# Kernel optimization log

Hardware: AMD Instinct MI355X
Metric: run time of the kernel (lower is better)

Reference implementation:

```python
import jax, jax.numpy as jnp
import numpy as np

G, N_PER, H, F_IN, E = 512, 128, 128, 133, 524288
K1, K2, K3 = 103, 83, 67  # ceil(0.8*n) chain: 128->103->83->67 (PyG TopKPooling ratio=0.8)
NEG = 0.01   # leaky_relu default slope
EPS = 1e-5   # BatchNorm eps


def setup_inputs() -> dict:
    key = jax.random.key(0)
    ks = jax.random.split(key, 16)
    e_per = E // G
    # edges are intra-graph: local endpoints + per-graph offset
    src_l = jax.random.randint(ks[0], (G, e_per), 0, N_PER)
    dst_l = jax.random.randint(ks[1], (G, e_per), 0, N_PER)
    off = (jnp.arange(G) * N_PER)[:, None]
    src = (src_l + off).reshape(-1).astype(jnp.int32)
    dst = (dst_l + off).reshape(-1).astype(jnp.int32)
    batch = jnp.repeat(jnp.arange(G, dtype=jnp.int32), N_PER)

    def rn(k, shape, scale=0.05):
        return jax.random.normal(k, shape, dtype=jnp.float32) * scale

    return dict(
        x=jax.random.normal(ks[2], (G * N_PER, F_IN), dtype=jnp.float32),
        src=src, dst=dst, batch=batch,
        W1=rn(ks[3], (F_IN, H)), b1=jnp.zeros((H,), jnp.float32),
        W2=rn(ks[4], (H, H)), b2=jnp.zeros((H,), jnp.float32),
        W3=rn(ks[5], (H, H)), b3=jnp.zeros((H,), jnp.float32),
        p1=rn(ks[6], (H,), 0.1), p2=rn(ks[7], (H,), 0.1), p3=rn(ks[8], (H,), 0.1),
        lin1_W=rn(ks[9], (2 * H, 1024)), lin1_b=jnp.zeros((1024,), jnp.float32),
        lin2_W=rn(ks[10], (1024, 64)), lin2_b=jnp.zeros((64,), jnp.float32),
        lin3_W=rn(ks[11], (64, 2)), lin3_b=jnp.zeros((2,), jnp.float32),
        bn1_g=jnp.ones((1024,), jnp.float32), bn1_b=jnp.zeros((1024,), jnp.float32),
        bn1_rm=jnp.zeros((1024,), jnp.float32), bn1_rv=jnp.ones((1024,), jnp.float32),
        bn2_g=jnp.ones((64,), jnp.float32), bn2_b=jnp.zeros((64,), jnp.float32),
        bn2_rm=jnp.zeros((64,), jnp.float32), bn2_rv=jnp.ones((64,), jnp.float32),
    )


def _gcn(x, W, b, src, dst, em, n_nodes):
    # GCNConv with self-loops & symmetric norm; em masks edges removed by pooling.
    deg = jax.ops.segment_sum(em, dst, num_segments=n_nodes) + 1.0  # +1 self loop
    dis = jax.lax.rsqrt(deg)
    h = x @ W
    coef = dis[src] * dis[dst] * em                      # [E]
    agg = jax.ops.segment_sum(h[src] * coef[:, None], dst, num_segments=n_nodes)
    return agg + h * (1.0 / deg)[:, None] + b            # self-loop term: deg_i^-1 * h_i


def _topk(x, p, src, dst, em, n_per, k):
    # TopKPooling: score = x@p/||p||, keep top-k per graph, gate by tanh(score).
    g = x.shape[0] // n_per
    score = (x @ p) / jnp.linalg.norm(p)                 # [g*n_per]
    vals, idx = jax.lax.top_k(score.reshape(g, n_per), k)  # [g,k]
    xk = jnp.take_along_axis(x.reshape(g, n_per, -1), idx[:, :, None], axis=1)
    x_new = (xk * jnp.tanh(vals)[:, :, None]).reshape(g * k, -1)
    # remap surviving edges; drop (mask) edges touching removed nodes
    remap = jnp.full((g * n_per,), -1, jnp.int32)
    gperm = (jnp.arange(g, dtype=jnp.int32)[:, None] * n_per + idx.astype(jnp.int32)).reshape(-1)
    remap = remap.at[gperm].set(jnp.arange(g * k, dtype=jnp.int32))
    s2, d2 = remap[src], remap[dst]
    ok = (s2 >= 0) & (d2 >= 0)
    return x_new, jnp.where(ok, s2, 0), jnp.where(ok, d2, 0), em * ok.astype(em.dtype)


def _readout(x, g):
    xg = x.reshape(g, -1, x.shape[-1])
    return jnp.concatenate([xg.max(axis=1), xg.mean(axis=1)], axis=-1)  # [g, 2H]


def _lrelu(v):
    return jax.nn.leaky_relu(v, NEG)


def _bn(v, gam, bet, rm, rv):  # eval-mode BatchNorm1d (running stats)
    return (v - rm) * jax.lax.rsqrt(rv + EPS) * gam + bet


def _forward(x, src, dst, W1, b1, W2, b2, W3, b3, p1, p2, p3,
             lin1_W, lin1_b, lin2_W, lin2_b, lin3_W, lin3_b,
             bn1_g, bn1_b, bn1_rm, bn1_rv, bn2_g, bn2_b, bn2_rm, bn2_rv):
    em = jnp.ones(src.shape, jnp.float32)
    h = _lrelu(_gcn(x, W1, b1, src, dst, em, G * N_PER))
    h, src, dst, em = _topk(h, p1, src, dst, em, N_PER, K1)
    r1 = _readout(h, G)
    h = _lrelu(_gcn(h, W2, b2, src, dst, em, G * K1))
    h, src, dst, em = _topk(h, p2, src, dst, em, K1, K2)
    r2 = _readout(h, G)
    h = _lrelu(_gcn(h, W3, b3, src, dst, em, G * K2))
    h, src, dst, em = _topk(h, p3, src, dst, em, K2, K3)
    r3 = _readout(h, G)
    z = r1 + r2 + r3                                      # [G, 2H]
    z = _bn(_lrelu(z @ lin1_W + lin1_b), bn1_g, bn1_b, bn1_rm, bn1_rv)
    z = _bn(_lrelu(z @ lin2_W + lin2_b), bn2_g, bn2_b, bn2_rm, bn2_rv)
    # dropout p=0.5 is identity in eval mode
    return z @ lin3_W + lin3_b                            # [G, num_classes]


def reference(x, src, dst, batch, W1, b1, W2, b2, W3, b3, p1, p2, p3,
              lin1_W, lin1_b, lin2_W, lin2_b, lin3_W, lin3_b,
              bn1_g, bn1_b, bn1_rm, bn1_rv, bn2_g, bn2_b, bn2_rm, bn2_rv):
    # batch is implicit in the regular [G, n_per] layout; kept for signature parity.
    return _forward(x, src, dst, W1, b1, W2, b2, W3, b3, p1, p2, p3,
                    lin1_W, lin1_b, lin2_W, lin2_b, lin3_W, lin3_b,
                    bn1_g, bn1_b, bn1_rm, bn1_rv, bn2_g, bn2_b, bn2_rm, bn2_rv)
```

## Files before the change

### kernel.cpp

```cpp
#include <hip/hip_runtime.h>

#define NEGS 0.01f
#define BNEPS 1e-5f

typedef short bf16x8 __attribute__((ext_vector_type(8)));
typedef float f32x4 __attribute__((ext_vector_type(4)));

__device__ __forceinline__ void split2(float v, short& hi, short& lo) {
    unsigned u = __float_as_uint(v);
    unsigned r = (u + 0x7FFFu + ((u >> 16) & 1u)) >> 16;
    hi = (short)r;
    float hf = __uint_as_float(r << 16);
    float l = v - hf;
    unsigned ul = __float_as_uint(l);
    lo = (short)((ul + 0x7FFFu + ((ul >> 16) & 1u)) >> 16);
}

__global__ __launch_bounds__(256) void split_all(
    const float* __restrict__ W1, const float* __restrict__ W2,
    const float* __restrict__ W3, const float* __restrict__ L1,
    short* __restrict__ h1, short* __restrict__ l1,
    short* __restrict__ h2, short* __restrict__ l2,
    short* __restrict__ h3, short* __restrict__ l3,
    short* __restrict__ h4, short* __restrict__ l4)
{
    int idx = blockIdx.x * 256 + threadIdx.x;
    const float* B; short *H, *L; int K, N, K32, loc;
    if (idx < 20480)      { B = W1; H = h1; L = l1; K = 133; N = 128;  K32 = 160; loc = idx; }
    else if (idx < 36864) { B = W2; H = h2; L = l2; K = 128; N = 128;  K32 = 128; loc = idx - 20480; }
    else if (idx < 53248) { B = W3; H = h3; L = l3; K = 128; N = 128;  K32 = 128; loc = idx - 36864; }
    else                  { B = L1; H = h4; L = l4; K = 256; N = 1024; K32 = 256; loc = idx - 53248; }
    int n = loc % N, k = loc / N;
    float v = (k < K) ? B[(long)k * N + n] : 0.f;
    short hi, lo; split2(v, hi, lo);
    H[(long)n * K32 + k] = hi;
    L[(long)n * K32 + k] = lo;
}

template<int KCH, int VEC, int EPI>
__global__ __launch_bounds__(256) void mfma_gemm(
    const float* __restrict__ A, const short* __restrict__ Bh_t,
    const short* __restrict__ Bl_t, float* __restrict__ C,
    int M, int N, int K,
    const float* __restrict__ bias, const float* __restrict__ bng,
    const float* __restrict__ bnb, const float* __restrict__ bnrm,
    const float* __restrict__ bnrv)
{
    constexpr int K32 = KCH * 32;
    __shared__ short Ahs[64 * 40], Als[64 * 40];
    __shared__ short Bhs[128 * 40], Bls[128 * 40];

    const int tid = threadIdx.x;
    const int bm = blockIdx.y * 64, bn = blockIdx.x * 128;
    const int lane = tid & 63, w = tid >> 6, wm = w >> 1, wn = w & 1;
    const int lm = lane & 15, lk = (lane >> 4) * 8;

    const int arow = tid >> 2, akl = (tid & 3) * 8;
    const int brow = tid & 127, bhl = tid >> 7;
    const short* bsrc = bhl ? Bl_t : Bh_t;
    short* bdst = bhl ? Bls : Bhs;

    const f32x4 zz = {0.f, 0.f, 0.f, 0.f};
    f32x4 acc[2][4];
#pragma unroll
    for (int i = 0; i < 2; ++i)
#pragma unroll
        for (int j = 0; j < 4; ++j) acc[i][j] = zz;

    for (int c = 0; c < KCH; ++c) {
        float av[8];
        if constexpr (VEC == 4) {
            const float4 v0 = *(const float4*)&A[(long)(bm + arow) * K + c * 32 + akl];
            const float4 v1 = *(const float4*)&A[(long)(bm + arow) * K + c * 32 + akl + 4];
            av[0] = v0.x; av[1] = v0.y; av[2] = v0.z; av[3] = v0.w;
            av[4] = v1.x; av[5] = v1.y; av[6] = v1.z; av[7] = v1.w;
        } else {
#pragma unroll
            for (int j = 0; j < 8; ++j) {
                int k = c * 32 + akl + j;
                av[j] = (k < K) ? A[(long)(bm + arow) * K + k] : 0.f;
            }
        }
        bf16x8 h8, l8;
#pragma unroll
        for (int j = 0; j < 8; ++j) { short h_, l_; split2(av[j], h_, l_); h8[j] = h_; l8[j] = l_; }
        *(bf16x8*)&Ahs[arow * 40 + akl] = h8;
        *(bf16x8*)&Als[arow * 40 + akl] = l8;
        const long bbase = (long)(bn + brow) * K32 + c * 32;
#pragma unroll
        for (int j = 0; j < 4; ++j)
            *(bf16x8*)&bdst[brow * 40 + j * 8] = *(const bf16x8*)&bsrc[bbase + j * 8];
        __syncthreads();

        bf16x8 ah0 = *(const bf16x8*)&Ahs[(wm * 32 + lm) * 40 + lk];
        bf16x8 ah1 = *(const bf16x8*)&Ahs[(wm * 32 + 16 + lm) * 40 + lk];
        bf16x8 al0 = *(const bf16x8*)&Als[(wm * 32 + lm) * 40 + lk];
        bf16x8 al1 = *(const bf16x8*)&Als[(wm * 32 + 16 + lm) * 40 + lk];
#pragma unroll
        for (int nt = 0; nt < 4; ++nt) {
            bf16x8 bh = *(const bf16x8*)&Bhs[(wn * 64 + nt * 16 + lm) * 40 + lk];
            bf16x8 bl = *(const bf16x8*)&Bls[(wn * 64 + nt * 16 + lm) * 40 + lk];
            acc[0][nt] = __builtin_amdgcn_mfma_f32_16x16x32_bf16(ah0, bh, acc[0][nt], 0, 0, 0);
            acc[1][nt] = __builtin_amdgcn_mfma_f32_16x16x32_bf16(ah1, bh, acc[1][nt], 0, 0, 0);
            acc[0][nt] = __builtin_amdgcn_mfma_f32_16x16x32_bf16(ah0, bl, acc[0][nt], 0, 0, 0);
            acc[1][nt] = __builtin_amdgcn_mfma_f32_16x16x32_bf16(ah1, bl, acc[1][nt], 0, 0, 0);
            acc[0][nt] = __builtin_amdgcn_mfma_f32_16x16x32_bf16(al0, bh, acc[0][nt], 0, 0, 0);
            acc[1][nt] = __builtin_amdgcn_mfma_f32_16x16x32_bf16(al1, bh, acc[1][nt], 0, 0, 0);
        }
        __syncthreads();
    }

#pragma unroll
    for (int mt = 0; mt < 2; ++mt) {
        int r0 = bm + wm * 32 + mt * 16 + (lane >> 4) * 4;
#pragma unroll
        for (int nt = 0; nt < 4; ++nt) {
            int col = bn + wn * 64 + nt * 16 + lm;
            float bi = 0.f, sc_ = 1.f, rm_ = 0.f, bb_ = 0.f;
            if (EPI == 1) {
                bi = bias[col];
                sc_ = (1.0f / sqrtf(bnrv[col] + BNEPS)) * bng[col];
                rm_ = bnrm[col]; bb_ = bnb[col];
            }
#pragma unroll
            for (int r = 0; r < 4; ++r) {
                float v = acc[mt][nt][r];
                if (EPI == 1) {
                    v += bi;
                    v = v >= 0.f ? v : NEGS * v;
                    v = (v - rm_) * sc_ + bb_;
                }
                C[(long)(r0 + r) * N + col] = v;
            }
        }
    }
}

template<int NC, int KK, bool FIRST, bool LAST, bool ACCUM>
__global__ __launch_bounds__(1024, 8) void gcn_topk(
    const float* __restrict__ h_pre,
    const int* __restrict__ srcIn, const int* __restrict__ dstIn,
    int* ePK,
    const float* __restrict__ bias, const float* __restrict__ p,
    float* __restrict__ x_new,
    float* __restrict__ z)
{
    __shared__ float h_s[NC][128];
    __shared__ float2 csr[1024];
    __shared__ int   head[NC];
    __shared__ float deg_s[NC], dis_s[NC], invd_s[NC];
    __shared__ float sc[128];
    __shared__ int   id[128];
    __shared__ float gate[KK];
    __shared__ float b_s[128], p_s[128];
    __shared__ int   remap_l[NC];
    __shared__ float pnorm;

    const int g = blockIdx.x, tid = threadIdx.x, lane = tid & 63;
    const float NINF = -__builtin_inff();
    constexpr int NITER = (NC + 7) / 8;

    int es_r, ed_r; bool live;
    {
        int eg = g * 1024 + tid;
        if (FIRST) { es_r = srcIn[eg] & 127; ed_r = dstIn[eg] & 127; live = true; }
        else       { int pk = ePK[eg]; es_r = pk & 127; ed_r = (pk >> 7) & 127; live = (pk >> 14) != 0; }
    }

    {
        const float4* hp = (const float4*)(h_pre + (long)g * NC * 128);
        float4* h4 = (float4*)&h_s[0][0];
        for (int i = tid; i < NC * 32; i += 1024) h4[i] = hp[i];
    }
    if (tid < 128) { b_s[tid] = bias[tid]; p_s[tid] = p[tid]; sc[tid] = 0.f; }
    for (int i = tid; i < NC; i += 1024) { deg_s[i] = 1.f; head[i] = 0; }
    __syncthreads();

    if (tid < 64) {
        float s = p_s[tid] * p_s[tid] + p_s[tid + 64] * p_s[tid + 64];
#pragma unroll
        for (int o = 32; o; o >>= 1) s += __shfl_xor(s, o, 64);
        if (tid == 0) pnorm = sqrtf(s);
    }
    if (live) {
        atomicAdd(&deg_s[ed_r], 1.0f);
        atomicAdd(&head[ed_r], 1);
    }
    __syncthreads();

    for (int i = tid; i < NC; i += 1024) {
        float d = deg_s[i];
        dis_s[i] = 1.0f / sqrtf(d);
        invd_s[i] = 1.0f / d;
    }
    if (tid < 64) {
        int c0 = head[tid];
        int c1 = (tid + 64 < NC) ? head[tid + 64] : 0;
        int s0 = c0, s1 = c1;
#pragma unroll
        for (int o = 1; o < 64; o <<= 1) { int t = __shfl_up(s0, o, 64); if (lane >= o) s0 += t; }
        int tot0 = __shfl(s0, 63, 64);
#pragma unroll
        for (int o = 1; o < 64; o <<= 1) { int t = __shfl_up(s1, o, 64); if (lane >= o) s1 += t; }
        s1 += tot0;
        head[tid] = s0 - c0;
        if (tid + 64 < NC) head[tid + 64] = s1 - c1;
    }
    __syncthreads();

    if (live) {
        int slot = atomicAdd(&head[ed_r], 1);
        csr[slot] = make_float2(__int_as_float(es_r), dis_s[es_r] * dis_s[ed_r]);
    }
    __syncthreads();

    float va[NITER];
    {
        const int f = tid & 127, grp = tid >> 7;
#pragma unroll
        for (int i = 0; i < NITER; ++i) {
            int nd = grp + i * 8;
            if (nd < NC) {
                int kb = nd ? head[nd - 1] : 0;
                int ke = head[nd];
                float acc = 0.f;
                for (int k = kb; k < ke; ++k) {
                    float2 rec = csr[k];
                    acc += h_s[__float_as_int(rec.x)][f] * rec.y;
                }
                float v = acc + h_s[nd][f] * invd_s[nd] + b_s[f];
                v = v >= 0.f ? v : NEGS * v;
                va[i] = v;
                float ps = v * p_s[f];
#pragma unroll
                for (int o = 32; o; o >>= 1) ps += __shfl_xor(ps, o, 64);
                if (lane == 0) atomicAdd(&sc[nd], ps);
            }
        }
    }
    __syncthreads();

    {
        const int f = tid & 127, grp = tid >> 7;
#pragma unroll
        for (int i = 0; i < NITER; ++i) {
            int nd = grp + i * 8;
            if (nd < NC) h_s[nd][f] = va[i];
        }
    }
    __syncthreads();

    if (tid < 128) {
        if (tid < NC) { sc[tid] = sc[tid] / pnorm; id[tid] = tid; }
        else          { sc[tid] = NINF; id[tid] = 0x7fffffff; }
    }
    __syncthreads();

    if (tid < 64) {
        for (int size = 2; size <= 128; size <<= 1) {
            for (int stride = size >> 1; stride > 0; stride >>= 1) {
                int i = 2 * stride * (tid / stride) + (tid % stride);
                int j = i + stride;
                float si_ = sc[i], sj_ = sc[j];
                int ii = id[i], ij = id[j];
                bool iFirst = (si_ > sj_) || (si_ == sj_ && ii < ij);
                bool descRegion = ((i & size) == 0);
                bool doSwap = descRegion ? !iFirst : iFirst;
                if (doSwap) { sc[i] = sj_; sc[j] = si_; id[i] = ij; id[j] = ii; }
                __asm__ volatile("" ::: "memory");
            }
        }
    }
    __syncthreads();

    for (int j = tid; j < KK; j += 1024) gate[j] = tanhf(sc[j]);
    if constexpr (!LAST) {
        for (int i = tid; i < NC; i += 1024) remap_l[i] = -1;
    }
    __syncthreads();
    if constexpr (!LAST) {
        for (int j = tid; j < KK; j += 1024) remap_l[id[j]] = j;
    }
    __syncthreads();

    if constexpr (!LAST) {
        int s2 = remap_l[es_r], d2 = remap_l[ed_r];
        bool ok = (s2 >= 0) && (d2 >= 0);
        int lv = (live && ok) ? 1 : 0;
        ePK[g * 1024 + tid] = (ok ? s2 : 0) | ((ok ? d2 : 0) << 7) | (lv << 14);
    }

    float* pmax = (float*)&csr[0];
    float* psum = pmax + 1024;
    {
        const int f = tid & 127, jj = tid >> 7;
        float rmx = NINF, rsm = 0.f;
        for (int j = jj; j < KK; j += 8) {
            float v = h_s[id[j]][f] * gate[j];
            if constexpr (!LAST) x_new[((long)g * KK + j) * 128 + f] = v;
            rmx = fmaxf(rmx, v);
            rsm += v;
        }
        pmax[jj * 128 + f] = rmx; psum[jj * 128 + f] = rsm;
    }
    __syncthreads();

    if (tid < 128) {
        float m = pmax[tid], s = psum[tid];
#pragma unroll
        for (int jj = 1; jj < 8; ++jj) { m = fmaxf(m, pmax[jj * 128 + tid]); s += psum[jj * 128 + tid]; }
        float mean = s / (float)KK;
        if constexpr (ACCUM) {
            z[g * 256 + tid] += m;
            z[g * 256 + 128 + tid] += mean;
        } else {
            z[g * 256 + tid] = m;
            z[g * 256 + 128 + tid] = mean;
        }
    }
}

__global__ __launch_bounds__(256) void mlp_tail(
    const float* __restrict__ t1,
    const float* __restrict__ W2, const float* __restrict__ b2v,
    const float* __restrict__ g2, const float* __restrict__ bb2,
    const float* __restrict__ rm2, const float* __restrict__ rv2,
    const float* __restrict__ W3, const float* __restrict__ b3v,
    float* __restrict__ out)
{
    __shared__ float t1s[1024];
    __shared__ float part[4][64];
    __shared__ float t2s[64];
    const int row = blockIdx.x, tid = threadIdx.x;

    for (int i = tid; i < 1024; i += 256) t1s[i] = t1[(long)row * 1024 + i];
    __syncthreads();

    int c = tid & 63, seg = tid >> 6;
    float s = 0.f;
    for (int k = seg * 256; k < seg * 256 + 256; ++k)
        s = fmaf(t1s[k], W2[k * 64 + c], s);
    part[seg][c] = s;
    __syncthreads();

    if (tid < 64) {
        float v = part[0][c] + part[1][c] + part[2][c] + part[3][c] + b2v[c];
        v = v >= 0.f ? v : NEGS * v;
        v = (v - rm2[c]) * (1.0f / sqrtf(rv2[c] + BNEPS)) * g2[c] + bb2[c];
        t2s[c] = v;
    }
    __syncthreads();

    if (tid < 128) {
        int cc = tid >> 6, k = tid & 63;
        float prod = t2s[k] * W3[k * 2 + cc];
#pragma unroll
        for (int o = 32; o; o >>= 1) prod += __shfl_xor(prod, o, 64);
        if (k == 0) out[row * 2 + cc] = prod + b3v[cc];
    }
}

extern "C" void kernel_launch(void* const* d_in, const int* in_sizes, int n_in,
                              void* d_out, int out_size, void* d_ws, size_t ws_size,
                              hipStream_t stream)
{
    const float* x    = (const float*)d_in[0];
    const int*   src  = (const int*)d_in[1];
    const int*   dst  = (const int*)d_in[2];
    const float* W1   = (const float*)d_in[4];
    const float* b1   = (const float*)d_in[5];
    const float* W2   = (const float*)d_in[6];
    const float* b2   = (const float*)d_in[7];
    const float* W3   = (const float*)d_in[8];
    const float* b3   = (const float*)d_in[9];
    const float* p1   = (const float*)d_in[10];
    const float* p2   = (const float*)d_in[11];
    const float* p3   = (const float*)d_in[12];
    const float* l1W  = (const float*)d_in[13];
    const float* l1b  = (const float*)d_in[14];
    const float* l2W  = (const float*)d_in[15];
    const float* l2b  = (const float*)d_in[16];
    const float* l3W  = (const float*)d_in[17];
    const float* l3b  = (const float*)d_in[18];
    const float* bn1g = (const float*)d_in[19];
    const float* bn1b = (const float*)d_in[20];
    const float* bn1rm= (const float*)d_in[21];
    const float* bn1rv= (const float*)d_in[22];
    const float* bn2g = (const float*)d_in[23];
    const float* bn2b = (const float*)d_in[24];
    const float* bn2rm= (const float*)d_in[25];
    const float* bn2rv= (const float*)d_in[26];
    float* out = (float*)d_out;

    float* ws = (float*)d_ws;
    size_t o = 0;
    float* h_pre = ws + o; o += 65536L * 128;
    float* x_cur = ws + o; o += 52736L * 128;
    float* z     = ws + o; o += 512L * 256;
    float* t1    = ws + o; o += 512L * 1024;
    int*   ePK   = (int*)(ws + o); o += 524288;
    short* sp = (short*)(ws + o);
    short* h1s = sp;
    short* l1s = h1s + 20480;
    short* h2s = l1s + 20480;
    short* l2s = h2s + 16384;
    short* h3s = l2s + 16384;
    short* l3s = h3s + 16384;
    short* h4s = l3s + 16384;
    short* l4s = h4s + 262144;

    split_all<<<1232, 256, 0, stream>>>(W1, W2, W3, l1W,
        h1s, l1s, h2s, l2s, h3s, l3s, h4s, l4s);

    mfma_gemm<5,1,0><<<dim3(1,1024), 256, 0, stream>>>(
        x, h1s, l1s, h_pre, 65536, 128, 133, nullptr, nullptr, nullptr, nullptr, nullptr);
    gcn_topk<128,103,true,false,false><<<512, 1024, 0, stream>>>(
        h_pre, src, dst, ePK, b1, p1, x_cur, z);

    mfma_gemm<4,4,0><<<dim3(1,824), 256, 0, stream>>>(
        x_cur, h2s, l2s, h_pre, 52736, 128, 128, nullptr, nullptr, nullptr, nullptr, nullptr);
    gcn_topk<103,83,false,false,true><<<512, 1024, 0, stream>>>(
        h_pre, nullptr, nullptr, ePK, b2, p2, x_cur, z);

    mfma_gemm<4,4,0><<<dim3(1,664), 256, 0, stream>>>(
        x_cur, h3s, l3s, h_pre, 42496, 128, 128, nullptr, nullptr, nullptr, nullptr, nullptr);
    gcn_topk<83,67,false,true,true><<<512, 1024, 0, stream>>>(
        h_pre, nullptr, nullptr, ePK, b3, p3, nullptr, z);

    mfma_gemm<8,4,1><<<dim3(8,8), 256, 0, stream>>>(
        z, h4s, l4s, t1, 512, 1024, 256, l1b, bn1g, bn1b, bn1rm, bn1rv);
    mlp_tail<<<512, 256, 0, stream>>>(
        t1, l2W, l2b, bn2g, bn2b, bn2rm, bn2rv, l3W, l3b, out);
}
```

Measured before the change: 296.5 us.

## Keep B weights resident in LDS and load A directly into MFMA registers; vectorize GCN aggregation

The GEMM is restructured so each block loads the whole split-bf16 B panel for its 128 columns into shared memory once. Each wave then reads its A rows straight from global memory into MFMA operand registers, which removes the per-K-chunk A staging through LDS and the two barriers per chunk, and the block tile grows to 128x128. In gcn_topk, the aggregation and pooling loops move to float4 per thread with 32 nodes in flight. The atomicAdd score update becomes a direct store, and the max/sum readout reduction reuses h_s. The costs are higher register pressure from 16 accumulators per wave, more LDS for the full K panel, and uncoalesced-per-lane global A loads.

```diff
diff --git a/kernel.cpp b/kernel.cpp
--- a/kernel.cpp
+++ b/kernel.cpp
@@ -37,87 +37,85 @@
     L[(long)n * K32 + k] = lo;
 }
 
-template<int KCH, int VEC, int EPI>
-__global__ __launch_bounds__(256) void mfma_gemm(
+template<int K, int K32, int EPI>
+__global__ __launch_bounds__(256) void gemm_bres(
     const float* __restrict__ A, const short* __restrict__ Bh_t,
-    const short* __restrict__ Bl_t, float* __restrict__ C,
-    int M, int N, int K,
+    const short* __restrict__ Bl_t, float* __restrict__ C, int N,
     const float* __restrict__ bias, const float* __restrict__ bng,
     const float* __restrict__ bnb, const float* __restrict__ bnrm,
     const float* __restrict__ bnrv)
 {
-    constexpr int K32 = KCH * 32;
-    __shared__ short Ahs[64 * 40], Als[64 * 40];
-    __shared__ short Bhs[128 * 40], Bls[128 * 40];
+    constexpr int KP = K32 + 8;
+    constexpr int NKS = K32 / 32;
+    __shared__ short Bhs[128 * KP];
+    __shared__ short Bls[128 * KP];
 
     const int tid = threadIdx.x;
-    const int bm = blockIdx.y * 64, bn = blockIdx.x * 128;
-    const int lane = tid & 63, w = tid >> 6, wm = w >> 1, wn = w & 1;
+    const int bm = blockIdx.x * 128, n0 = blockIdx.y * 128;
+    const int lane = tid & 63, w = tid >> 6;
     const int lm = lane & 15, lk = (lane >> 4) * 8;
 
-    const int arow = tid >> 2, akl = (tid & 3) * 8;
-    const int brow = tid & 127, bhl = tid >> 7;
-    const short* bsrc = bhl ? Bl_t : Bh_t;
-    short* bdst = bhl ? Bls : Bhs;
+    for (int i = tid; i < 128 * (K32 / 8); i += 256) {
+        int n = i / (K32 / 8), kb = (i % (K32 / 8)) * 8;
+        *(bf16x8*)&Bhs[n * KP + kb] = *(const bf16x8*)&Bh_t[(long)(n0 + n) * K32 + kb];
+        *(bf16x8*)&Bls[n * KP + kb] = *(const bf16x8*)&Bl_t[(long)(n0 + n) * K32 + kb];
+    }
+    __syncthreads();
 
     const f32x4 zz = {0.f, 0.f, 0.f, 0.f};
-    f32x4 acc[2][4];
+    f32x4 acc[2][8];
 #pragma unroll
     for (int i = 0; i < 2; ++i)
 #pragma unroll
-        for (int j = 0; j < 4; ++j) acc[i][j] = zz;
-
-    for (int c = 0; c < KCH; ++c) {
-        float av[8];
-        if constexpr (VEC == 4) {
-            const float4 v0 = *(const float4*)&A[(long)(bm + arow) * K + c * 32 + akl];
-            const float4 v1 = *(const float4*)&A[(long)(bm + arow) * K + c * 32 + akl + 4];
-            av[0] = v0.x; av[1] = v0.y; av[2] = v0.z; av[3] = v0.w;
-            av[4] = v1.x; av[5] = v1.y; av[6] = v1.z; av[7] = v1.w;
-        } else {
+        for (int j = 0; j < 8; ++j) acc[i][j] = zz;
+
+    const int r0 = bm + w * 32;
+    for (int ks = 0; ks < NKS; ++ks) {
+        const int k0 = ks * 32 + lk;
+        bf16x8 ah[2], al[2];
+#pragma unroll
+        for (int mt = 0; mt < 2; ++mt) {
+            const long rowb = (long)(r0 + mt * 16 + lm) * K;
+            float av[8];
+            if constexpr (K % 4 == 0) {
+                const float4 v0 = *(const float4*)&A[rowb + k0];
+                const float4 v1 = *(const float4*)&A[rowb + k0 + 4];
+                av[0] = v0.x; av[1] = v0.y; av[2] = v0.z; av[3] = v0.w;
+                av[4] = v1.x; av[5] = v1.y; av[6] = v1.z; av[7] = v1.w;
+            } else {
+#pragma unroll
+                for (int j = 0; j < 8; ++j) {
+                    int kk = k0 + j;
+                    av[j] = (kk < K) ? A[rowb + kk] : 0.f;
+                }
+            }
 #pragma unroll
             for (int j = 0; j < 8; ++j) {
-                int k = c * 32 + akl + j;
-                av[j] = (k < K) ? A[(long)(bm + arow) * K + k] : 0.f;
-            }
-        }
-        bf16x8 h8, l8;
-#pragma unroll
-        for (int j = 0; j < 8; ++j) { short h_, l_; split2(av[j], h_, l_); h8[j] = h_; l8[j] = l_; }
-        *(bf16x8*)&Ahs[arow * 40 + akl] = h8;
-        *(bf16x8*)&Als[arow * 40 + akl] = l8;
-        const long bbase = (long)(bn + brow) * K32 + c * 32;
-#pragma unroll
-        for (int j = 0; j < 4; ++j)
-            *(bf16x8*)&bdst[brow * 40 + j * 8] = *(const bf16x8*)&bsrc[bbase + j * 8];
-        __syncthreads();
-
-        bf16x8 ah0 = *(const bf16x8*)&Ahs[(wm * 32 + lm) * 40 + lk];
-        bf16x8 ah1 = *(const bf16x8*)&Ahs[(wm * 32 + 16 + lm) * 40 + lk];
-        bf16x8 al0 = *(const bf16x8*)&Als[(wm * 32 + lm) * 40 + lk];
-        bf16x8 al1 = *(const bf16x8*)&Als[(wm * 32 + 16 + lm) * 40 + lk];
-#pragma unroll
-        for (int nt = 0; nt < 4; ++nt) {
-            bf16x8 bh = *(const bf16x8*)&Bhs[(wn * 64 + nt * 16 + lm) * 40 + lk];
-            bf16x8 bl = *(const bf16x8*)&Bls[(wn * 64 + nt * 16 + lm) * 40 + lk];
-            acc[0][nt] = __builtin_amdgcn_mfma_f32_16x16x32_bf16(ah0, bh, acc[0][nt], 0, 0, 0);
-            acc[1][nt] = __builtin_amdgcn_mfma_f32_16x16x32_bf16(ah1, bh, acc[1][nt], 0, 0, 0);
-            acc[0][nt] = __builtin_amdgcn_mfma_f32_16x16x32_bf16(ah0, bl, acc[0][nt], 0, 0, 0);
-            acc[1][nt] = __builtin_amdgcn_mfma_f32_16x16x32_bf16(ah1, bl, acc[1][nt], 0, 0, 0);
-            acc[0][nt] = __builtin_amdgcn_mfma_f32_16x16x32_bf16(al0, bh, acc[0][nt], 0, 0, 0);
-            acc[1][nt] = __builtin_amdgcn_mfma_f32_16x16x32_bf16(al1, bh, acc[1][nt], 0, 0, 0);
-        }
-        __syncthreads();
+                short h_, l_; split2(av[j], h_, l_);
+                ah[mt][j] = h_; al[mt][j] = l_;
+            }
+        }
+#pragma unroll
+        for (int nt = 0; nt < 8; ++nt) {
+            bf16x8 bh = *(const bf16x8*)&Bhs[(nt * 16 + lm) * KP + k0];
+            bf16x8 bl = *(const bf16x8*)&Bls[(nt * 16 + lm) * KP + k0];
+#pragma unroll
+            for (int mt = 0; mt < 2; ++mt) {
+                acc[mt][nt] = __builtin_amdgcn_mfma_f32_16x16x32_bf16(ah[mt], bh, acc[mt][nt], 0, 0, 0);
+                acc[mt][nt] = __builtin_amdgcn_mfma_f32_16x16x32_bf16(ah[mt], bl, acc[mt][nt], 0, 0, 0);
+                acc[mt][nt] = __builtin_amdgcn_mfma_f32_16x16x32_bf16(al[mt], bh, acc[mt][nt], 0, 0, 0);
+            }
+        }
     }
 
 #pragma unroll
     for (int mt = 0; mt < 2; ++mt) {
-        int r0 = bm + wm * 32 + mt * 16 + (lane >> 4) * 4;
-#pragma unroll
-        for (int nt = 0; nt < 4; ++nt) {
-            int col = bn + wn * 64 + nt * 16 + lm;
+        const int row0 = r0 + mt * 16 + (lane >> 4) * 4;
+#pragma unroll
+        for (int nt = 0; nt < 8; ++nt) {
+            const int col = n0 + nt * 16 + lm;
             float bi = 0.f, sc_ = 1.f, rm_ = 0.f, bb_ = 0.f;
-            if (EPI == 1) {
+            if constexpr (EPI == 1) {
                 bi = bias[col];
                 sc_ = (1.0f / sqrtf(bnrv[col] + BNEPS)) * bng[col];
                 rm_ = bnrm[col]; bb_ = bnb[col];
@@ -125,12 +123,12 @@
 #pragma unroll
             for (int r = 0; r < 4; ++r) {
                 float v = acc[mt][nt][r];
-                if (EPI == 1) {
+                if constexpr (EPI == 1) {
                     v += bi;
                     v = v >= 0.f ? v : NEGS * v;
                     v = (v - rm_) * sc_ + bb_;
                 }
-                C[(long)(r0 + r) * N + col] = v;
+                C[(long)(row0 + r) * N + col] = v;
             }
         }
     }
@@ -157,8 +155,10 @@
     __shared__ float pnorm;
 
     const int g = blockIdx.x, tid = threadIdx.x, lane = tid & 63;
+    const int f4 = (tid & 31) * 4;
+    const int grp = tid >> 5;
     const float NINF = -__builtin_inff();
-    constexpr int NITER = (NC + 7) / 8;
+    constexpr int NIT4 = (NC + 31) / 32;
 
     int es_r, ed_r; bool live;
     {
@@ -172,7 +172,7 @@
         float4* h4 = (float4*)&h_s[0][0];
         for (int i = tid; i < NC * 32; i += 1024) h4[i] = hp[i];
     }
-    if (tid < 128) { b_s[tid] = bias[tid]; p_s[tid] = p[tid]; sc[tid] = 0.f; }
+    if (tid < 128) { b_s[tid] = bias[tid]; p_s[tid] = p[tid]; }
     for (int i = tid; i < NC; i += 1024) { deg_s[i] = 1.f; head[i] = 0; }
     __syncthreads();
 
@@ -214,39 +214,51 @@
     }
     __syncthreads();
 
-    float va[NITER];
-    {
-        const int f = tid & 127, grp = tid >> 7;
-#pragma unroll
-        for (int i = 0; i < NITER; ++i) {
-            int nd = grp + i * 8;
-            if (nd < NC) {
-                int kb = nd ? head[nd - 1] : 0;
-                int ke = head[nd];
-                float acc = 0.f;
-                for (int k = kb; k < ke; ++k) {
-                    float2 rec = csr[k];
-                    acc += h_s[__float_as_int(rec.x)][f] * rec.y;
-                }
-                float v = acc + h_s[nd][f] * invd_s[nd] + b_s[f];
-                v = v >= 0.f ? v : NEGS * v;
-                va[i] = v;
-                float ps = v * p_s[f];
-#pragma unroll
-                for (int o = 32; o; o >>= 1) ps += __shfl_xor(ps, o, 64);
-                if (lane == 0) atomicAdd(&sc[nd], ps);
-            }
-        }
-    }
-    __syncthreads();
-
-    {
-        const int f = tid & 127, grp = tid >> 7;
-#pragma unroll
-        for (int i = 0; i < NITER; ++i) {
-            int nd = grp + i * 8;
-            if (nd < NC) h_s[nd][f] = va[i];
-        }
+    const float4 p4 = *(const float4*)&p_s[f4];
+    const float4 b4 = *(const float4*)&b_s[f4];
+    float4 va[NIT4];
+#pragma unroll
+    for (int i = 0; i < NIT4; ++i) {
+        int nd = grp + i * 32;
+        if ((NC & 31) == 0 || nd < NC) {
+            int kb = nd ? head[nd - 1] : 0;
+            int ke = head[nd];
+            float4 acc = make_float4(0.f, 0.f, 0.f, 0.f);
+            for (int k = kb; k < ke; ++k) {
+                float2 rec = csr[k];
+                const float4 hv = *(const float4*)&h_s[__float_as_int(rec.x)][f4];
+                acc.x = fmaf(hv.x, rec.y, acc.x);
+                acc.y = fmaf(hv.y, rec.y, acc.y);
+                acc.z = fmaf(hv.z, rec.y, acc.z);
+                acc.w = fmaf(hv.w, rec.y, acc.w);
+            }
+            const float4 h0 = *(const float4*)&h_s[nd][f4];
+            const float iv = invd_s[nd];
+            float4 v;
+            v.x = acc.x + h0.x * iv + b4.x;
+            v.y = acc.y + h0.y * iv + b4.y;
+            v.z = acc.z + h0.z * iv + b4.z;
+            v.w = acc.w + h0.w * iv + b4.w;
+            v.x = v.x >= 0.f ? v.x : NEGS * v.x;
+            v.y = v.y >= 0.f ? v.y : NEGS * v.y;
+            v.z = v.z >= 0.f ? v.z : NEGS * v.z;
+            v.w = v.w >= 0.f ? v.w : NEGS * v.w;
+            va[i] = v;
+            float ps = v.x * p4.x + v.y * p4.y + v.z * p4.z + v.w * p4.w;
+            ps += __shfl_xor(ps, 16, 64);
+            ps += __shfl_xor(ps, 8, 64);
+            ps += __shfl_xor(ps, 4, 64);
+            ps += __shfl_xor(ps, 2, 64);
+            ps += __shfl_xor(ps, 1, 64);
+            if ((tid & 31) == 0) sc[nd] = ps;
+        }
+    }
+    __syncthreads();
+
+#pragma unroll
+    for (int i = 0; i < NIT4; ++i) {
+        int nd = grp + i * 32;
+        if ((NC & 31) == 0 || nd < NC) *(float4*)&h_s[nd][f4] = va[i];
     }
     __syncthreads();
 
@@ -290,25 +302,41 @@
         ePK[g * 1024 + tid] = (ok ? s2 : 0) | ((ok ? d2 : 0) << 7) | (lv << 14);
     }
 
-    float* pmax = (float*)&csr[0];
-    float* psum = pmax + 1024;
     {
-        const int f = tid & 127, jj = tid >> 7;
-        float rmx = NINF, rsm = 0.f;
-        for (int j = jj; j < KK; j += 8) {
-            float v = h_s[id[j]][f] * gate[j];
-            if constexpr (!LAST) x_new[((long)g * KK + j) * 128 + f] = v;
-            rmx = fmaxf(rmx, v);
-            rsm += v;
-        }
-        pmax[jj * 128 + f] = rmx; psum[jj * 128 + f] = rsm;
+        const int jj = tid >> 5;
+        float4 rmx = make_float4(NINF, NINF, NINF, NINF);
+        float4 rsm = make_float4(0.f, 0.f, 0.f, 0.f);
+        for (int j = jj; j < KK; j += 32) {
+            const float gt = gate[j];
+            const float4 hv = *(const float4*)&h_s[id[j]][f4];
+            float4 v;
+            v.x = hv.x * gt; v.y = hv.y * gt; v.z = hv.z * gt; v.w = hv.w * gt;
+            if constexpr (!LAST) *(float4*)&x_new[((long)g * KK + j) * 128 + f4] = v;
+            rmx.x = fmaxf(rmx.x, v.x); rmx.y = fmaxf(rmx.y, v.y);
+            rmx.z = fmaxf(rmx.z, v.z); rmx.w = fmaxf(rmx.w, v.w);
+            rsm.x += v.x; rsm.y += v.y; rsm.z += v.z; rsm.w += v.w;
+        }
+        rmx.x = fmaxf(rmx.x, __shfl_xor(rmx.x, 32, 64));
+        rmx.y = fmaxf(rmx.y, __shfl_xor(rmx.y, 32, 64));
+        rmx.z = fmaxf(rmx.z, __shfl_xor(rmx.z, 32, 64));
+        rmx.w = fmaxf(rmx.w, __shfl_xor(rmx.w, 32, 64));
+        rsm.x += __shfl_xor(rsm.x, 32, 64);
+        rsm.y += __shfl_xor(rsm.y, 32, 64);
+        rsm.z += __shfl_xor(rsm.z, 32, 64);
+        rsm.w += __shfl_xor(rsm.w, 32, 64);
+        __syncthreads();
+        if (lane < 32) {
+            const int w = tid >> 6;
+            *(float4*)&h_s[w][f4] = rmx;
+            *(float4*)&h_s[16 + w][f4] = rsm;
+        }
     }
     __syncthreads();
 
     if (tid < 128) {
-        float m = pmax[tid], s = psum[tid];
-#pragma unroll
-        for (int jj = 1; jj < 8; ++jj) { m = fmaxf(m, pmax[jj * 128 + tid]); s += psum[jj * 128 + tid]; }
+        float m = h_s[0][tid], s = h_s[16][tid];
+#pragma unroll
+        for (int q = 1; q < 16; ++q) { m = fmaxf(m, h_s[q][tid]); s += h_s[16 + q][tid]; }
         float mean = s / (float)KK;
         if constexpr (ACCUM) {
             z[g * 256 + tid] += m;
@@ -412,23 +440,23 @@
     split_all<<<1232, 256, 0, stream>>>(W1, W2, W3, l1W,
         h1s, l1s, h2s, l2s, h3s, l3s, h4s, l4s);
 
-    mfma_gemm<5,1,0><<<dim3(1,1024), 256, 0, stream>>>(
-        x, h1s, l1s, h_pre, 65536, 128, 133, nullptr, nullptr, nullptr, nullptr, nullptr);
+    gemm_bres<133,160,0><<<dim3(512,1), 256, 0, stream>>>(
+        x, h1s, l1s, h_pre, 128, nullptr, nullptr, nullptr, nullptr, nullptr);
     gcn_topk<128,103,true,false,false><<<512, 1024, 0, stream>>>(
         h_pre, src, dst, ePK, b1, p1, x_cur, z);
 
-    mfma_gemm<4,4,0><<<dim3(1,824), 256, 0, stream>>>(
-        x_cur, h2s, l2s, h_pre, 52736, 128, 128, nullptr, nullptr, nullptr, nullptr, nullptr);
+    gemm_bres<128,128,0><<<dim3(412,1), 256, 0, stream>>>(
+        x_cur, h2s, l2s, h_pre, 128, nullptr, nullptr, nullptr, nullptr, nullptr);
     gcn_topk<103,83,false,false,true><<<512, 1024, 0, stream>>>(
         h_pre, nullptr, nullptr, ePK, b2, p2, x_cur, z);
 
-    mfma_gemm<4,4,0><<<dim3(1,664), 256, 0, stream>>>(
-        x_cur, h3s, l3s, h_pre, 42496, 128, 128, nullptr, nullptr, nullptr, nullptr, nullptr);
+    gemm_bres<128,128,0><<<dim3(332,1), 256, 0, stream>>>(
+        x_cur, h3s, l3s, h_pre, 128, nullptr, nullptr, nullptr, nullptr, nullptr);
     gcn_topk<83,67,false,true,true><<<512, 1024, 0, stream>>>(
         h_pre, nullptr, nullptr, ePK, b3, p3, nullptr, z);
 
-    mfma_gemm<8,4,1><<<dim3(8,8), 256, 0, stream>>>(
-        z, h4s, l4s, t1, 512, 1024, 256, l1b, bn1g, bn1b, bn1rm, bn1rv);
+    gemm_bres<256,256,1><<<dim3(4,8), 256, 0, stream>>>(
+        z, h4s, l4s, t1, 1024, l1b, bn1g, bn1b, bn1rm, bn1rv);
     mlp_tail<<<512, 256, 0, stream>>>(
         t1, l2W, l2b, bn2g, bn2b, bn2rm, bn2rv, l3W, l3b, out);
 }
```

Result: faster. 262.9 us (-11.3%).
